# Optimization experiments

Hardware: AMD Instinct MI355X
Metric: run time of the kernel (lower is better)

Reference implementation:

```python
import jax, jax.numpy as jnp
import numpy as np

H = 4096      # hidden_size
F = 14336     # intermediate_size (ffn)
GS = 64       # HQQ group_size along axis 0 (output rows)
NB = 4        # nbits
T = 512       # tokens routed to this expert


def _make_qlinear(key, N, K):
    """Quantized weight of logical shape (N, K) = (out, in), HQQ axis=0 groups."""
    k1, k2, k3 = jax.random.split(key, 3)
    W_q = jax.random.randint(k1, (N, K), 0, 2 ** NB, dtype=jnp.int32)
    scale = jax.random.uniform(k2, (N // GS, K), dtype=jnp.float32) * 0.02 + 1e-3
    zero = jax.random.uniform(k3, (N // GS, K), dtype=jnp.float32) * (2.0 ** (NB - 1))
    return W_q, scale, zero


def setup_inputs() -> dict:
    key = jax.random.key(0)
    kx, k1, k2, k3 = jax.random.split(key, 4)
    w1_q, w1_scale, w1_zero = _make_qlinear(k1, F, H)  # gate proj
    w2_q, w2_scale, w2_zero = _make_qlinear(k2, H, F)  # down proj
    w3_q, w3_scale, w3_zero = _make_qlinear(k3, F, H)  # up proj
    hidden_states = jax.random.normal(kx, (T, H), dtype=jnp.float32)
    return dict(hidden_states=hidden_states,
                w1_q=w1_q, w1_scale=w1_scale, w1_zero=w1_zero,
                w2_q=w2_q, w2_scale=w2_scale, w2_zero=w2_zero,
                w3_q=w3_q, w3_scale=w3_scale, w3_zero=w3_zero)


def _dequant(W_q, scale, zero):
    # W[n, k] = (W_q[n, k] - zero[n // GS, k]) * scale[n // GS, k]
    N, K = W_q.shape
    Wf = W_q.reshape(N // GS, GS, K).astype(scale.dtype)
    return ((Wf - zero[:, None, :]) * scale[:, None, :]).reshape(N, K)


def reference(hidden_states,
              w1_q, w1_scale, w1_zero,
              w2_q, w2_scale, w2_zero,
              w3_q, w3_scale, w3_zero):
    gate = hidden_states @ _dequant(w1_q, w1_scale, w1_zero).T  # [T, F]
    up = hidden_states @ _dequant(w3_q, w3_scale, w3_zero).T    # [T, F]
    inter = jax.nn.silu(gate) * up                               # [T, F]
    return inter @ _dequant(w2_q, w2_scale, w2_zero).T           # [T, H]
```

## Files before the change

### kernel.cpp

```cpp
#include <hip/hip_runtime.h>
#include <stdint.h>

typedef __bf16 bf16;
typedef __attribute__((ext_vector_type(8))) bf16 bf16x8;
typedef __attribute__((ext_vector_type(4))) bf16 bf16x4;
typedef __attribute__((ext_vector_type(4))) float f32x4;

#define T_DIM 512
#define H_DIM 4096
#define F_DIM 14336

__device__ __forceinline__ int swz(int r, int c) {
    return r * 64 + (c ^ ((r & 7) << 3));
}

__device__ __forceinline__ int xcd_remap(int d, int chunk) {
    return (d & 7) * chunk + (d >> 3);
}

__device__ __forceinline__ void barrier_nodrain() {
    __builtin_amdgcn_sched_barrier(0);
    asm volatile("s_waitcnt lgkmcnt(0)\n\ts_barrier" ::: "memory");
    __builtin_amdgcn_sched_barrier(0);
}

__global__ void cvt_x_kernel(const float* __restrict__ x, bf16* __restrict__ xb) {
    int i = (blockIdx.x * 256 + threadIdx.x) * 4;
    float4 v = *(const float4*)(x + i);
    bf16x4 o = {(bf16)v.x, (bf16)v.y, (bf16)v.z, (bf16)v.w};
    *(bf16x4*)(xb + i) = o;
}

__global__ __launch_bounds__(256, 3)
void gemm_gateup(const bf16* __restrict__ A,
                 const int* __restrict__ Wq1, const float* __restrict__ Sc1,
                 const float* __restrict__ Zr1,
                 const int* __restrict__ Wq3, const float* __restrict__ Sc3,
                 const float* __restrict__ Zr3,
                 bf16* __restrict__ inter) {
    constexpr int KD = H_DIM;
    constexpr int NT = KD / 64;
    __shared__ __align__(16) bf16 As[2][128 * 64];
    __shared__ __align__(16) bf16 Bs1[2][32 * 64];
    __shared__ __align__(16) bf16 Bs3[2][32 * 64];

    const int l    = xcd_remap(blockIdx.x, 224);
    const int bx   = l & 3;
    const int by   = l >> 2;
    const int tid  = threadIdx.x;
    const int lane = tid & 63;
    const int wid  = tid >> 6;
    const int wm   = wid >> 1, wn = wid & 1;
    const int lr   = lane & 15;
    const int lk   = (lane >> 4) * 8;
    const int m0   = bx * 128;
    const int n0   = by * 32;
    const int grp  = n0 >> 6;

    const int a_r = tid >> 2;
    const int a_c = (tid & 3) * 8;
    const int b_r = (tid >> 4) * 2;
    const int b_c = (tid & 15) * 4;

    f32x4 acc1[4], acc3[4];
    const f32x4 zf = {0.f, 0.f, 0.f, 0.f};
#pragma unroll
    for (int i = 0; i < 4; i++) { acc1[i] = zf; acc3[i] = zf; }

    bf16x8 areg[4];
    int4   q1r[2], q3r[2];
    float4 s1r, z1r, s3r, z3r;

#define STAGE(K0)                                                                 \
    {                                                                             \
        _Pragma("unroll")                                                         \
        for (int p = 0; p < 2; p++)                                               \
            _Pragma("unroll")                                                     \
            for (int h = 0; h < 2; h++)                                           \
                areg[p * 2 + h] = *(const bf16x8*)(A + (size_t)(m0 + a_r + 64 * p) * KD + (K0) + a_c + 32 * h); \
        _Pragma("unroll")                                                         \
        for (int i = 0; i < 2; i++) {                                             \
            q1r[i] = *(const int4*)(Wq1 + (size_t)(n0 + b_r + i) * KD + (K0) + b_c); \
            q3r[i] = *(const int4*)(Wq3 + (size_t)(n0 + b_r + i) * KD + (K0) + b_c); \
        }                                                                         \
        s1r = *(const float4*)(Sc1 + (size_t)grp * KD + (K0) + b_c);              \
        z1r = *(const float4*)(Zr1 + (size_t)grp * KD + (K0) + b_c);              \
        s3r = *(const float4*)(Sc3 + (size_t)grp * KD + (K0) + b_c);              \
        z3r = *(const float4*)(Zr3 + (size_t)grp * KD + (K0) + b_c);              \
    }

#define WLDS(nb)                                                                  \
    {                                                                             \
        _Pragma("unroll")                                                         \
        for (int p = 0; p < 2; p++)                                               \
            _Pragma("unroll")                                                     \
            for (int h = 0; h < 2; h++)                                           \
                *(bf16x8*)&As[nb][swz(a_r + 64 * p, a_c + 32 * h)] = areg[p * 2 + h]; \
        float4 n1, n3;                                                            \
        n1.x = -z1r.x * s1r.x; n1.y = -z1r.y * s1r.y;                             \
        n1.z = -z1r.z * s1r.z; n1.w = -z1r.w * s1r.w;                             \
        n3.x = -z3r.x * s3r.x; n3.y = -z3r.y * s3r.y;                             \
        n3.z = -z3r.z * s3r.z; n3.w = -z3r.w * s3r.w;                             \
        _Pragma("unroll")                                                         \
        for (int i = 0; i < 2; i++) {                                             \
            bf16x4 v;                                                             \
            v[0] = (bf16)fmaf((float)q1r[i].x, s1r.x, n1.x);                      \
            v[1] = (bf16)fmaf((float)q1r[i].y, s1r.y, n1.y);                      \
            v[2] = (bf16)fmaf((float)q1r[i].z, s1r.z, n1.z);                      \
            v[3] = (bf16)fmaf((float)q1r[i].w, s1r.w, n1.w);                      \
            *(bf16x4*)&Bs1[nb][swz(b_r + i, b_c)] = v;                            \
            bf16x4 u;                                                             \
            u[0] = (bf16)fmaf((float)q3r[i].x, s3r.x, n3.x);                      \
            u[1] = (bf16)fmaf((float)q3r[i].y, s3r.y, n3.y);                      \
            u[2] = (bf16)fmaf((float)q3r[i].z, s3r.z, n3.z);                      \
            u[3] = (bf16)fmaf((float)q3r[i].w, s3r.w, n3.w);                      \
            *(bf16x4*)&Bs3[nb][swz(b_r + i, b_c)] = u;                            \
        }                                                                         \
    }

    STAGE(0);
    WLDS(0);
    STAGE(64);
    barrier_nodrain();

    for (int t = 0; t < NT; ++t) {
        const int cur = t & 1;
#pragma unroll
        for (int kk = 0; kk < 2; kk++) {
            bf16x8 af[4], b1, b3;
#pragma unroll
            for (int mi = 0; mi < 4; mi++)
                af[mi] = *(const bf16x8*)&As[cur][swz(wm * 64 + mi * 16 + lr, kk * 32 + lk)];
            b1 = *(const bf16x8*)&Bs1[cur][swz(wn * 16 + lr, kk * 32 + lk)];
            b3 = *(const bf16x8*)&Bs3[cur][swz(wn * 16 + lr, kk * 32 + lk)];
#pragma unroll
            for (int mi = 0; mi < 4; mi++) {
                acc1[mi] = __builtin_amdgcn_mfma_f32_16x16x32_bf16(af[mi], b1, acc1[mi], 0, 0, 0);
                acc3[mi] = __builtin_amdgcn_mfma_f32_16x16x32_bf16(af[mi], b3, acc3[mi], 0, 0, 0);
            }
        }
        if (t + 1 < NT) {
            WLDS(cur ^ 1);
            if (t + 2 < NT) STAGE((t + 2) * 64);
            barrier_nodrain();
        }
    }
#undef STAGE
#undef WLDS

    const int orow = (lane >> 4) * 4;
#pragma unroll
    for (int mi = 0; mi < 4; mi++) {
#pragma unroll
        for (int r = 0; r < 4; r++) {
            int m = m0 + wm * 64 + mi * 16 + orow + r;
            int c = n0 + wn * 16 + lr;
            float g = acc1[mi][r];
            float u = acc3[mi][r];
            float s = g / (1.0f + __expf(-g));
            inter[(size_t)m * F_DIM + c] = (bf16)(s * u);
        }
    }
}

template<int SPLITK>
__global__ __launch_bounds__(256, 4)
void gemm_down(const bf16* __restrict__ A, const int* __restrict__ Wq,
               const float* __restrict__ Sc, const float* __restrict__ Zr,
               float* __restrict__ partials) {
    constexpr int KD = F_DIM;
    constexpr int KC = KD / SPLITK;
    constexpr int NT = KC / 64;
    __shared__ __align__(16) bf16 As[2][128 * 64];
    __shared__ __align__(16) bf16 Bs[2][32 * 64];

    const int l    = xcd_remap(blockIdx.x, 64 * SPLITK);
    const int bx   = l & 3;
    const int by   = (l >> 2) & 127;
    const int bz   = l >> 9;
    const int tid  = threadIdx.x;
    const int lane = tid & 63;
    const int wid  = tid >> 6;
    const int wm   = wid >> 1, wn = wid & 1;
    const int lr   = lane & 15;
    const int lk   = (lane >> 4) * 8;
    const int m0   = bx * 128;
    const int n0   = by * 32;
    const int grp  = n0 >> 6;
    const int kbeg = bz * KC;

    const int a_r = tid >> 2;
    const int a_c = (tid & 3) * 8;
    const int b_r = (tid >> 4) * 2;
    const int b_c = (tid & 15) * 4;

    f32x4 acc[4];
    const f32x4 zf = {0.f, 0.f, 0.f, 0.f};
#pragma unroll
    for (int i = 0; i < 4; i++) acc[i] = zf;

    bf16x8 areg[4];
    int4   qr[2];
    float4 sr, zr;

#define STAGE(K0)                                                                 \
    {                                                                             \
        _Pragma("unroll")                                                         \
        for (int p = 0; p < 2; p++)                                               \
            _Pragma("unroll")                                                     \
            for (int h = 0; h < 2; h++)                                           \
                areg[p * 2 + h] = *(const bf16x8*)(A + (size_t)(m0 + a_r + 64 * p) * KD + kbeg + (K0) + a_c + 32 * h); \
        _Pragma("unroll")                                                         \
        for (int i = 0; i < 2; i++)                                               \
            qr[i] = *(const int4*)(Wq + (size_t)(n0 + b_r + i) * KD + kbeg + (K0) + b_c); \
        sr = *(const float4*)(Sc + (size_t)grp * KD + kbeg + (K0) + b_c);         \
        zr = *(const float4*)(Zr + (size_t)grp * KD + kbeg + (K0) + b_c);         \
    }

#define WLDS(nb)                                                                  \
    {                                                                             \
        _Pragma("unroll")                                                         \
        for (int p = 0; p < 2; p++)                                               \
            _Pragma("unroll")                                                     \
            for (int h = 0; h < 2; h++)                                           \
                *(bf16x8*)&As[nb][swz(a_r + 64 * p, a_c + 32 * h)] = areg[p * 2 + h]; \
        float4 nz;                                                                \
        nz.x = -zr.x * sr.x; nz.y = -zr.y * sr.y;                                 \
        nz.z = -zr.z * sr.z; nz.w = -zr.w * sr.w;                                 \
        _Pragma("unroll")                                                         \
        for (int i = 0; i < 2; i++) {                                             \
            bf16x4 v;                                                             \
            v[0] = (bf16)fmaf((float)qr[i].x, sr.x, nz.x);                        \
            v[1] = (bf16)fmaf((float)qr[i].y, sr.y, nz.y);                        \
            v[2] = (bf16)fmaf((float)qr[i].z, sr.z, nz.z);                        \
            v[3] = (bf16)fmaf((float)qr[i].w, sr.w, nz.w);                        \
            *(bf16x4*)&Bs[nb][swz(b_r + i, b_c)] = v;                             \
        }                                                                         \
    }

    STAGE(0);
    WLDS(0);
    STAGE(64);
    barrier_nodrain();

    for (int t = 0; t < NT; ++t) {
        const int cur = t & 1;
#pragma unroll
        for (int kk = 0; kk < 2; kk++) {
            bf16x8 af[4], bfr;
#pragma unroll
            for (int mi = 0; mi < 4; mi++)
                af[mi] = *(const bf16x8*)&As[cur][swz(wm * 64 + mi * 16 + lr, kk * 32 + lk)];
            bfr = *(const bf16x8*)&Bs[cur][swz(wn * 16 + lr, kk * 32 + lk)];
#pragma unroll
            for (int mi = 0; mi < 4; mi++)
                acc[mi] = __builtin_amdgcn_mfma_f32_16x16x32_bf16(af[mi], bfr, acc[mi], 0, 0, 0);
        }
        if (t + 1 < NT) {
            WLDS(cur ^ 1);
            if (t + 2 < NT) STAGE((t + 2) * 64);
            barrier_nodrain();
        }
    }
#undef STAGE
#undef WLDS

    float* po = partials + (size_t)bz * T_DIM * H_DIM;
    const int orow = (lane >> 4) * 4;
#pragma unroll
    for (int mi = 0; mi < 4; mi++) {
#pragma unroll
        for (int r = 0; r < 4; r++) {
            int m = m0 + wm * 64 + mi * 16 + orow + r;
            int c = n0 + wn * 16 + lr;
            po[(size_t)m * H_DIM + c] = acc[mi][r];
        }
    }
}

template<int S>
__global__ void reduce_kernel(const float* __restrict__ partials, float* __restrict__ out) {
    size_t i = ((size_t)blockIdx.x * 256 + threadIdx.x) * 4;
    f32x4 a = *(const f32x4*)(partials + i);
#pragma unroll
    for (int s = 1; s < S; s++)
        a += *(const f32x4*)(partials + (size_t)s * T_DIM * H_DIM + i);
    *(f32x4*)(out + i) = a;
}

extern "C" void kernel_launch(void* const* d_in, const int* in_sizes, int n_in,
                              void* d_out, int out_size, void* d_ws, size_t ws_size,
                              hipStream_t stream) {
    const float* x   = (const float*)d_in[0];
    const int*   w1q = (const int*)d_in[1];
    const float* w1s = (const float*)d_in[2];
    const float* w1z = (const float*)d_in[3];
    const int*   w2q = (const int*)d_in[4];
    const float* w2s = (const float*)d_in[5];
    const float* w2z = (const float*)d_in[6];
    const int*   w3q = (const int*)d_in[7];
    const float* w3s = (const float*)d_in[8];
    const float* w3z = (const float*)d_in[9];

    bf16*  xb    = (bf16*)d_ws;
    bf16*  inter = xb + (size_t)T_DIM * H_DIM;
    float* parts = (float*)(inter + (size_t)T_DIM * F_DIM);

    const size_t base   = (size_t)T_DIM * H_DIM * 2 + (size_t)T_DIM * F_DIM * 2;
    const size_t pbytes = (size_t)T_DIM * H_DIM * 4;

    cvt_x_kernel<<<dim3(2048), dim3(256), 0, stream>>>(x, xb);

    gemm_gateup<<<dim3(1792), dim3(256), 0, stream>>>(
        xb, w1q, w1s, w1z, w3q, w3s, w3z, inter);

    if (ws_size >= base + 4 * pbytes) {
        gemm_down<4><<<dim3(2048), dim3(256), 0, stream>>>(inter, w2q, w2s, w2z, parts);
        reduce_kernel<4><<<dim3(2048), dim3(256), 0, stream>>>(parts, (float*)d_out);
    } else if (ws_size >= base + 2 * pbytes) {
        gemm_down<2><<<dim3(1024), dim3(256), 0, stream>>>(inter, w2q, w2s, w2z, parts);
        reduce_kernel<2><<<dim3(2048), dim3(256), 0, stream>>>(parts, (float*)d_out);
    } else {
        gemm_down<1><<<dim3(512), dim3(256), 0, stream>>>(inter, w2q, w2s, w2z, parts);
        reduce_kernel<1><<<dim3(2048), dim3(256), 0, stream>>>(parts, (float*)d_out);
    }
}
```

Baseline: 446.4 us.

## Pre-tile activations and DMA A tiles directly to LDS with deeper weight prefetch

The bf16 activations and the intermediate tensor are now written in a pre-swizzled 128x64 tile layout, so each A tile can be copied straight into LDS with global_load_lds 16-byte DMA instead of going through registers. Weight loads are double-buffered in registers, prefetching two K-tiles ahead, and barriers wait on partial vmcnt counts. The aim is to cut VGPR staging and LDS write instructions for A and to hide more global-load latency. The cost is a strict dependence on the custom layout and on hand-counted vmcnt values, which are fragile if the compiler reorders loads.

```diff
diff --git a/kernel.cpp b/kernel.cpp
--- a/kernel.cpp
+++ b/kernel.cpp
@@ -18,18 +18,30 @@
     return (d & 7) * chunk + (d >> 3);
 }
 
-__device__ __forceinline__ void barrier_nodrain() {
-    __builtin_amdgcn_sched_barrier(0);
-    asm volatile("s_waitcnt lgkmcnt(0)\n\ts_barrier" ::: "memory");
-    __builtin_amdgcn_sched_barrier(0);
-}
-
-__global__ void cvt_x_kernel(const float* __restrict__ x, bf16* __restrict__ xb) {
+__device__ __forceinline__ void dma16(const void* g, void* l) {
+    __builtin_amdgcn_global_load_lds(
+        (const __attribute__((address_space(1))) void*)g,
+        (__attribute__((address_space(3))) void*)l, 16, 0, 0);
+}
+
+#define BARRIER_VM(N)                                                        \
+    {                                                                        \
+        __builtin_amdgcn_sched_barrier(0);                                   \
+        asm volatile("s_waitcnt vmcnt(" #N ") lgkmcnt(0)\n\ts_barrier" ::: "memory"); \
+        __builtin_amdgcn_sched_barrier(0);                                   \
+    }
+
+__global__ void cvt_x_kernel(const float* __restrict__ x, bf16* __restrict__ xbt) {
     int i = (blockIdx.x * 256 + threadIdx.x) * 4;
+    int m = i >> 12;
+    int c = i & 4095;
     float4 v = *(const float4*)(x + i);
     bf16x4 o = {(bf16)v.x, (bf16)v.y, (bf16)v.z, (bf16)v.w};
-    *(bf16x4*)(xb + i) = o;
-}
+    int p = m >> 7, rm = m & 127, kt = c >> 6, kc = c & 63;
+    *(bf16x4*)(xbt + (size_t)(p * 64 + kt) * 8192 + swz(rm, kc)) = o;
+}
+
+struct WSet { int4 q1[2], q3[2]; float4 s1, z1, s3, z3; };
 
 __global__ __launch_bounds__(256, 3)
 void gemm_gateup(const bf16* __restrict__ A,
@@ -57,115 +69,153 @@
     const int n0   = by * 32;
     const int grp  = n0 >> 6;
 
-    const int a_r = tid >> 2;
-    const int a_c = (tid & 3) * 8;
     const int b_r = (tid >> 4) * 2;
     const int b_c = (tid & 15) * 4;
 
+    const char*  atile = (const char*)A + (size_t)bx * 64 * 16384;
+    const size_t dmaoff = (size_t)wid * 4096 + lane * 16;
+
+    const int*   q1B = Wq1 + (size_t)(n0 + b_r) * KD + b_c;
+    const int*   q3B = Wq3 + (size_t)(n0 + b_r) * KD + b_c;
+    const float* s1B = Sc1 + (size_t)grp * KD + b_c;
+    const float* z1B = Zr1 + (size_t)grp * KD + b_c;
+    const float* s3B = Sc3 + (size_t)grp * KD + b_c;
+    const float* z3B = Zr3 + (size_t)grp * KD + b_c;
+
     f32x4 acc1[4], acc3[4];
     const f32x4 zf = {0.f, 0.f, 0.f, 0.f};
 #pragma unroll
     for (int i = 0; i < 4; i++) { acc1[i] = zf; acc3[i] = zf; }
 
-    bf16x8 areg[4];
-    int4   q1r[2], q3r[2];
-    float4 s1r, z1r, s3r, z3r;
-
-#define STAGE(K0)                                                                 \
-    {                                                                             \
-        _Pragma("unroll")                                                         \
-        for (int p = 0; p < 2; p++)                                               \
-            _Pragma("unroll")                                                     \
-            for (int h = 0; h < 2; h++)                                           \
-                areg[p * 2 + h] = *(const bf16x8*)(A + (size_t)(m0 + a_r + 64 * p) * KD + (K0) + a_c + 32 * h); \
-        _Pragma("unroll")                                                         \
-        for (int i = 0; i < 2; i++) {                                             \
-            q1r[i] = *(const int4*)(Wq1 + (size_t)(n0 + b_r + i) * KD + (K0) + b_c); \
-            q3r[i] = *(const int4*)(Wq3 + (size_t)(n0 + b_r + i) * KD + (K0) + b_c); \
-        }                                                                         \
-        s1r = *(const float4*)(Sc1 + (size_t)grp * KD + (K0) + b_c);              \
-        z1r = *(const float4*)(Zr1 + (size_t)grp * KD + (K0) + b_c);              \
-        s3r = *(const float4*)(Sc3 + (size_t)grp * KD + (K0) + b_c);              \
-        z3r = *(const float4*)(Zr3 + (size_t)grp * KD + (K0) + b_c);              \
-    }
-
-#define WLDS(nb)                                                                  \
-    {                                                                             \
-        _Pragma("unroll")                                                         \
-        for (int p = 0; p < 2; p++)                                               \
-            _Pragma("unroll")                                                     \
-            for (int h = 0; h < 2; h++)                                           \
-                *(bf16x8*)&As[nb][swz(a_r + 64 * p, a_c + 32 * h)] = areg[p * 2 + h]; \
-        float4 n1, n3;                                                            \
-        n1.x = -z1r.x * s1r.x; n1.y = -z1r.y * s1r.y;                             \
-        n1.z = -z1r.z * s1r.z; n1.w = -z1r.w * s1r.w;                             \
-        n3.x = -z3r.x * s3r.x; n3.y = -z3r.y * s3r.y;                             \
-        n3.z = -z3r.z * s3r.z; n3.w = -z3r.w * s3r.w;                             \
-        _Pragma("unroll")                                                         \
-        for (int i = 0; i < 2; i++) {                                             \
-            bf16x4 v;                                                             \
-            v[0] = (bf16)fmaf((float)q1r[i].x, s1r.x, n1.x);                      \
-            v[1] = (bf16)fmaf((float)q1r[i].y, s1r.y, n1.y);                      \
-            v[2] = (bf16)fmaf((float)q1r[i].z, s1r.z, n1.z);                      \
-            v[3] = (bf16)fmaf((float)q1r[i].w, s1r.w, n1.w);                      \
-            *(bf16x4*)&Bs1[nb][swz(b_r + i, b_c)] = v;                            \
-            bf16x4 u;                                                             \
-            u[0] = (bf16)fmaf((float)q3r[i].x, s3r.x, n3.x);                      \
-            u[1] = (bf16)fmaf((float)q3r[i].y, s3r.y, n3.y);                      \
-            u[2] = (bf16)fmaf((float)q3r[i].z, s3r.z, n3.z);                      \
-            u[3] = (bf16)fmaf((float)q3r[i].w, s3r.w, n3.w);                      \
-            *(bf16x4*)&Bs3[nb][swz(b_r + i, b_c)] = u;                            \
-        }                                                                         \
-    }
-
-    STAGE(0);
-    WLDS(0);
-    STAGE(64);
-    barrier_nodrain();
-
-    for (int t = 0; t < NT; ++t) {
-        const int cur = t & 1;
-#pragma unroll
-        for (int kk = 0; kk < 2; kk++) {
-            bf16x8 af[4], b1, b3;
-#pragma unroll
-            for (int mi = 0; mi < 4; mi++)
-                af[mi] = *(const bf16x8*)&As[cur][swz(wm * 64 + mi * 16 + lr, kk * 32 + lk)];
-            b1 = *(const bf16x8*)&Bs1[cur][swz(wn * 16 + lr, kk * 32 + lk)];
-            b3 = *(const bf16x8*)&Bs3[cur][swz(wn * 16 + lr, kk * 32 + lk)];
-#pragma unroll
-            for (int mi = 0; mi < 4; mi++) {
-                acc1[mi] = __builtin_amdgcn_mfma_f32_16x16x32_bf16(af[mi], b1, acc1[mi], 0, 0, 0);
-                acc3[mi] = __builtin_amdgcn_mfma_f32_16x16x32_bf16(af[mi], b3, acc3[mi], 0, 0, 0);
+    WSet sA, sB;
+
+#define GU_DMA(TILE, nb)                                                      \
+    {                                                                         \
+        const char* _s = atile + (size_t)(TILE) * 16384 + dmaoff;             \
+        char* _d = (char*)&As[nb][0] + wid * 4096;                            \
+        _Pragma("unroll")                                                     \
+        for (int j = 0; j < 4; j++) dma16(_s + j * 1024, _d + j * 1024);      \
+    }
+
+#define GU_STAGE(S, K0)                                                       \
+    {                                                                         \
+        _Pragma("unroll")                                                     \
+        for (int i = 0; i < 2; i++) {                                         \
+            S.q1[i] = *(const int4*)(q1B + (size_t)i * KD + (K0));            \
+            S.q3[i] = *(const int4*)(q3B + (size_t)i * KD + (K0));            \
+        }                                                                     \
+        S.s1 = *(const float4*)(s1B + (K0));                                  \
+        S.z1 = *(const float4*)(z1B + (K0));                                  \
+        S.s3 = *(const float4*)(s3B + (K0));                                  \
+        S.z3 = *(const float4*)(z3B + (K0));                                  \
+    }
+
+#define GU_WLDS(S, nb)                                                        \
+    {                                                                         \
+        float4 n1, n3;                                                        \
+        n1.x = -S.z1.x * S.s1.x; n1.y = -S.z1.y * S.s1.y;                     \
+        n1.z = -S.z1.z * S.s1.z; n1.w = -S.z1.w * S.s1.w;                     \
+        n3.x = -S.z3.x * S.s3.x; n3.y = -S.z3.y * S.s3.y;                     \
+        n3.z = -S.z3.z * S.s3.z; n3.w = -S.z3.w * S.s3.w;                     \
+        _Pragma("unroll")                                                     \
+        for (int i = 0; i < 2; i++) {                                         \
+            bf16x4 v;                                                         \
+            v[0] = (bf16)fmaf((float)S.q1[i].x, S.s1.x, n1.x);                \
+            v[1] = (bf16)fmaf((float)S.q1[i].y, S.s1.y, n1.y);                \
+            v[2] = (bf16)fmaf((float)S.q1[i].z, S.s1.z, n1.z);                \
+            v[3] = (bf16)fmaf((float)S.q1[i].w, S.s1.w, n1.w);                \
+            *(bf16x4*)&Bs1[nb][swz(b_r + i, b_c)] = v;                        \
+            bf16x4 u;                                                         \
+            u[0] = (bf16)fmaf((float)S.q3[i].x, S.s3.x, n3.x);                \
+            u[1] = (bf16)fmaf((float)S.q3[i].y, S.s3.y, n3.y);                \
+            u[2] = (bf16)fmaf((float)S.q3[i].z, S.s3.z, n3.z);                \
+            u[3] = (bf16)fmaf((float)S.q3[i].w, S.s3.w, n3.w);                \
+            *(bf16x4*)&Bs3[nb][swz(b_r + i, b_c)] = u;                        \
+        }                                                                     \
+    }
+
+#define GU_MFMA(nb)                                                           \
+    {                                                                         \
+        _Pragma("unroll")                                                     \
+        for (int kk = 0; kk < 2; kk++) {                                      \
+            bf16x8 af[4], b1, b3;                                             \
+            _Pragma("unroll")                                                 \
+            for (int mi = 0; mi < 4; mi++)                                    \
+                af[mi] = *(const bf16x8*)&As[nb][swz(wm * 64 + mi * 16 + lr, kk * 32 + lk)]; \
+            b1 = *(const bf16x8*)&Bs1[nb][swz(wn * 16 + lr, kk * 32 + lk)];   \
+            b3 = *(const bf16x8*)&Bs3[nb][swz(wn * 16 + lr, kk * 32 + lk)];   \
+            _Pragma("unroll")                                                 \
+            for (int mi = 0; mi < 4; mi++) {                                  \
+                acc1[mi] = __builtin_amdgcn_mfma_f32_16x16x32_bf16(af[mi], b1, acc1[mi], 0, 0, 0); \
+                acc3[mi] = __builtin_amdgcn_mfma_f32_16x16x32_bf16(af[mi], b3, acc3[mi], 0, 0, 0); \
+            }                                                                 \
+        }                                                                     \
+    }
+
+    GU_STAGE(sA, 0);
+    GU_DMA(0, 0);
+    GU_WLDS(sA, 0);
+    GU_STAGE(sB, 64);
+    GU_STAGE(sA, 128);
+    BARRIER_VM(16);
+
+    for (int t = 0; t < NT; t += 2) {
+        if (t + 1 < NT) GU_DMA(t + 1, 1);
+        __builtin_amdgcn_sched_barrier(0);
+        GU_MFMA(0);
+        if (t + 1 < NT) {
+            GU_WLDS(sB, 1);
+            if (t + 3 < NT) {
+                GU_STAGE(sB, (t + 3) * 64);
+                BARRIER_VM(8);
+            } else {
+                BARRIER_VM(0);
             }
         }
-        if (t + 1 < NT) {
-            WLDS(cur ^ 1);
-            if (t + 2 < NT) STAGE((t + 2) * 64);
-            barrier_nodrain();
-        }
-    }
-#undef STAGE
-#undef WLDS
+        const int u = t + 1;
+        if (u < NT) {
+            if (u + 1 < NT) GU_DMA(u + 1, 0);
+            __builtin_amdgcn_sched_barrier(0);
+            GU_MFMA(1);
+            if (u + 1 < NT) {
+                GU_WLDS(sA, 0);
+                if (u + 3 < NT) {
+                    GU_STAGE(sA, (u + 3) * 64);
+                    BARRIER_VM(8);
+                } else {
+                    BARRIER_VM(0);
+                }
+            }
+        }
+    }
+#undef GU_DMA
+#undef GU_STAGE
+#undef GU_WLDS
+#undef GU_MFMA
 
     const int orow = (lane >> 4) * 4;
+    const int cg   = n0 + wn * 16 + lr;
+    const int kt   = cg >> 6, kc = cg & 63;
+    bf16* itile = inter + (size_t)(bx * 224 + kt) * 8192;
 #pragma unroll
     for (int mi = 0; mi < 4; mi++) {
 #pragma unroll
         for (int r = 0; r < 4; r++) {
-            int m = m0 + wm * 64 + mi * 16 + orow + r;
-            int c = n0 + wn * 16 + lr;
+            int rm = (wm * 64 + mi * 16 + orow + r) & 127;
             float g = acc1[mi][r];
             float u = acc3[mi][r];
             float s = g / (1.0f + __expf(-g));
-            inter[(size_t)m * F_DIM + c] = (bf16)(s * u);
-        }
-    }
-}
+            itile[swz(rm, kc)] = (bf16)(s * u);
+        }
+    }
+}
+
+struct WSetD { int4 q[2]; float4 s, z; };
 
 template<int SPLITK>
 __global__ __launch_bounds__(256, 4)
-void gemm_down(const bf16* __restrict__ A, const int* __restrict__ Wq,
+void gemm_down(const bf16* __restrict__ A,
+               const int* __restrict__ Wq,
                const float* __restrict__ Sc, const float* __restrict__ Zr,
                float* __restrict__ partials) {
     constexpr int KD = F_DIM;
@@ -187,83 +237,114 @@
     const int m0   = bx * 128;
     const int n0   = by * 32;
     const int grp  = n0 >> 6;
-    const int kbeg = bz * KC;
-
-    const int a_r = tid >> 2;
-    const int a_c = (tid & 3) * 8;
+    const int kt0  = bz * (KC / 64);
+
     const int b_r = (tid >> 4) * 2;
     const int b_c = (tid & 15) * 4;
 
+    const char*  atile = (const char*)A + (size_t)(bx * 224 + kt0) * 16384;
+    const size_t dmaoff = (size_t)wid * 4096 + lane * 16;
+    const int    kbeg  = bz * KC;
+
+    const int*   qB = Wq + (size_t)(n0 + b_r) * KD + kbeg + b_c;
+    const float* sB_ = Sc + (size_t)grp * KD + kbeg + b_c;
+    const float* zB_ = Zr + (size_t)grp * KD + kbeg + b_c;
+
     f32x4 acc[4];
     const f32x4 zf = {0.f, 0.f, 0.f, 0.f};
 #pragma unroll
     for (int i = 0; i < 4; i++) acc[i] = zf;
 
-    bf16x8 areg[4];
-    int4   qr[2];
-    float4 sr, zr;
-
-#define STAGE(K0)                                                                 \
-    {                                                                             \
-        _Pragma("unroll")                                                         \
-        for (int p = 0; p < 2; p++)                                               \
-            _Pragma("unroll")                                                     \
-            for (int h = 0; h < 2; h++)                                           \
-                areg[p * 2 + h] = *(const bf16x8*)(A + (size_t)(m0 + a_r + 64 * p) * KD + kbeg + (K0) + a_c + 32 * h); \
-        _Pragma("unroll")                                                         \
-        for (int i = 0; i < 2; i++)                                               \
-            qr[i] = *(const int4*)(Wq + (size_t)(n0 + b_r + i) * KD + kbeg + (K0) + b_c); \
-        sr = *(const float4*)(Sc + (size_t)grp * KD + kbeg + (K0) + b_c);         \
-        zr = *(const float4*)(Zr + (size_t)grp * KD + kbeg + (K0) + b_c);         \
-    }
-
-#define WLDS(nb)                                                                  \
-    {                                                                             \
-        _Pragma("unroll")                                                         \
-        for (int p = 0; p < 2; p++)                                               \
-            _Pragma("unroll")                                                     \
-            for (int h = 0; h < 2; h++)                                           \
-                *(bf16x8*)&As[nb][swz(a_r + 64 * p, a_c + 32 * h)] = areg[p * 2 + h]; \
-        float4 nz;                                                                \
-        nz.x = -zr.x * sr.x; nz.y = -zr.y * sr.y;                                 \
-        nz.z = -zr.z * sr.z; nz.w = -zr.w * sr.w;                                 \
-        _Pragma("unroll")                                                         \
-        for (int i = 0; i < 2; i++) {                                             \
-            bf16x4 v;                                                             \
-            v[0] = (bf16)fmaf((float)qr[i].x, sr.x, nz.x);                        \
-            v[1] = (bf16)fmaf((float)qr[i].y, sr.y, nz.y);                        \
-            v[2] = (bf16)fmaf((float)qr[i].z, sr.z, nz.z);                        \
-            v[3] = (bf16)fmaf((float)qr[i].w, sr.w, nz.w);                        \
-            *(bf16x4*)&Bs[nb][swz(b_r + i, b_c)] = v;                             \
-        }                                                                         \
-    }
-
-    STAGE(0);
-    WLDS(0);
-    STAGE(64);
-    barrier_nodrain();
-
-    for (int t = 0; t < NT; ++t) {
-        const int cur = t & 1;
-#pragma unroll
-        for (int kk = 0; kk < 2; kk++) {
-            bf16x8 af[4], bfr;
-#pragma unroll
-            for (int mi = 0; mi < 4; mi++)
-                af[mi] = *(const bf16x8*)&As[cur][swz(wm * 64 + mi * 16 + lr, kk * 32 + lk)];
-            bfr = *(const bf16x8*)&Bs[cur][swz(wn * 16 + lr, kk * 32 + lk)];
-#pragma unroll
-            for (int mi = 0; mi < 4; mi++)
-                acc[mi] = __builtin_amdgcn_mfma_f32_16x16x32_bf16(af[mi], bfr, acc[mi], 0, 0, 0);
-        }
+    WSetD sA, sB;
+
+#define GD_DMA(TILE, nb)                                                      \
+    {                                                                         \
+        const char* _s = atile + (size_t)(TILE) * 16384 + dmaoff;             \
+        char* _d = (char*)&As[nb][0] + wid * 4096;                            \
+        _Pragma("unroll")                                                     \
+        for (int j = 0; j < 4; j++) dma16(_s + j * 1024, _d + j * 1024);      \
+    }
+
+#define GD_STAGE(S, K0)                                                       \
+    {                                                                         \
+        _Pragma("unroll")                                                     \
+        for (int i = 0; i < 2; i++)                                           \
+            S.q[i] = *(const int4*)(qB + (size_t)i * KD + (K0));              \
+        S.s = *(const float4*)(sB_ + (K0));                                   \
+        S.z = *(const float4*)(zB_ + (K0));                                   \
+    }
+
+#define GD_WLDS(S, nb)                                                        \
+    {                                                                         \
+        float4 nz;                                                            \
+        nz.x = -S.z.x * S.s.x; nz.y = -S.z.y * S.s.y;                         \
+        nz.z = -S.z.z * S.s.z; nz.w = -S.z.w * S.s.w;                         \
+        _Pragma("unroll")                                                     \
+        for (int i = 0; i < 2; i++) {                                         \
+            bf16x4 v;                                                         \
+            v[0] = (bf16)fmaf((float)S.q[i].x, S.s.x, nz.x);                  \
+            v[1] = (bf16)fmaf((float)S.q[i].y, S.s.y, nz.y);                  \
+            v[2] = (bf16)fmaf((float)S.q[i].z, S.s.z, nz.z);                  \
+            v[3] = (bf16)fmaf((float)S.q[i].w, S.s.w, nz.w);                  \
+            *(bf16x4*)&Bs[nb][swz(b_r + i, b_c)] = v;                         \
+        }                                                                     \
+    }
+
+#define GD_MFMA(nb)                                                           \
+    {                                                                         \
+        _Pragma("unroll")                                                     \
+        for (int kk = 0; kk < 2; kk++) {                                      \
+            bf16x8 af[4], bfr;                                                \
+            _Pragma("unroll")                                                 \
+            for (int mi = 0; mi < 4; mi++)                                    \
+                af[mi] = *(const bf16x8*)&As[nb][swz(wm * 64 + mi * 16 + lr, kk * 32 + lk)]; \
+            bfr = *(const bf16x8*)&Bs[nb][swz(wn * 16 + lr, kk * 32 + lk)];   \
+            _Pragma("unroll")                                                 \
+            for (int mi = 0; mi < 4; mi++)                                    \
+                acc[mi] = __builtin_amdgcn_mfma_f32_16x16x32_bf16(af[mi], bfr, acc[mi], 0, 0, 0); \
+        }                                                                     \
+    }
+
+    GD_STAGE(sA, 0);
+    GD_DMA(0, 0);
+    GD_WLDS(sA, 0);
+    GD_STAGE(sB, 64);
+    GD_STAGE(sA, 128);
+    BARRIER_VM(8);
+
+    for (int t = 0; t < NT; t += 2) {
+        if (t + 1 < NT) GD_DMA(t + 1, 1);
+        __builtin_amdgcn_sched_barrier(0);
+        GD_MFMA(0);
         if (t + 1 < NT) {
-            WLDS(cur ^ 1);
-            if (t + 2 < NT) STAGE((t + 2) * 64);
-            barrier_nodrain();
-        }
-    }
-#undef STAGE
-#undef WLDS
+            GD_WLDS(sB, 1);
+            if (t + 3 < NT) {
+                GD_STAGE(sB, (t + 3) * 64);
+                BARRIER_VM(4);
+            } else {
+                BARRIER_VM(0);
+            }
+        }
+        const int u = t + 1;
+        if (u < NT) {
+            if (u + 1 < NT) GD_DMA(u + 1, 0);
+            __builtin_amdgcn_sched_barrier(0);
+            GD_MFMA(1);
+            if (u + 1 < NT) {
+                GD_WLDS(sA, 0);
+                if (u + 3 < NT) {
+                    GD_STAGE(sA, (u + 3) * 64);
+                    BARRIER_VM(4);
+                } else {
+                    BARRIER_VM(0);
+                }
+            }
+        }
+    }
+#undef GD_DMA
+#undef GD_STAGE
+#undef GD_WLDS
+#undef GD_MFMA
 
     float* po = partials + (size_t)bz * T_DIM * H_DIM;
     const int orow = (lane >> 4) * 4;
```

Result: no change. 453.7 us (+1.6%).

## Pre-tile activations into swizzled tiles and read A fragments directly from global

Applied to the files above, without the earlier changes.

The bf16 activations and the intermediate tensor are now written into a pre-tiled, pre-swizzled layout of 128x64 tiles. Both GEMMs then load their A fragments directly from global memory instead of staging them through shared memory. This removes the A tile staging (global to register to LDS) and shrinks LDS use, which could raise occupancy. The trade-off is that every wave issues direct global loads in the inner loop with no LDS reuse across the two N-waves, so the kernel relies on L1/L2 caching and the loads may stall the MFMA pipeline.

```diff
diff --git a/kernel.cpp b/kernel.cpp
--- a/kernel.cpp
+++ b/kernel.cpp
@@ -24,11 +24,14 @@
     __builtin_amdgcn_sched_barrier(0);
 }
 
-__global__ void cvt_x_kernel(const float* __restrict__ x, bf16* __restrict__ xb) {
+__global__ void cvt_x_kernel(const float* __restrict__ x, bf16* __restrict__ xbt) {
     int i = (blockIdx.x * 256 + threadIdx.x) * 4;
+    int m = i >> 12;
+    int c = i & 4095;
     float4 v = *(const float4*)(x + i);
     bf16x4 o = {(bf16)v.x, (bf16)v.y, (bf16)v.z, (bf16)v.w};
-    *(bf16x4*)(xb + i) = o;
+    int p = m >> 7, rm = m & 127, kt = c >> 6, kc = c & 63;
+    *(bf16x4*)(xbt + (size_t)(p * 64 + kt) * 8192 + swz(rm, kc)) = o;
 }
 
 __global__ __launch_bounds__(256, 3)
@@ -40,7 +43,6 @@
                  bf16* __restrict__ inter) {
     constexpr int KD = H_DIM;
     constexpr int NT = KD / 64;
-    __shared__ __align__(16) bf16 As[2][128 * 64];
     __shared__ __align__(16) bf16 Bs1[2][32 * 64];
     __shared__ __align__(16) bf16 Bs3[2][32 * 64];
 
@@ -53,31 +55,24 @@
     const int wm   = wid >> 1, wn = wid & 1;
     const int lr   = lane & 15;
     const int lk   = (lane >> 4) * 8;
-    const int m0   = bx * 128;
     const int n0   = by * 32;
     const int grp  = n0 >> 6;
 
-    const int a_r = tid >> 2;
-    const int a_c = (tid & 3) * 8;
     const int b_r = (tid >> 4) * 2;
     const int b_c = (tid & 15) * 4;
 
+    const bf16* at0 = A + (size_t)bx * 64 * 8192;
+
     f32x4 acc1[4], acc3[4];
     const f32x4 zf = {0.f, 0.f, 0.f, 0.f};
 #pragma unroll
     for (int i = 0; i < 4; i++) { acc1[i] = zf; acc3[i] = zf; }
 
-    bf16x8 areg[4];
     int4   q1r[2], q3r[2];
     float4 s1r, z1r, s3r, z3r;
 
 #define STAGE(K0)                                                                 \
     {                                                                             \
-        _Pragma("unroll")                                                         \
-        for (int p = 0; p < 2; p++)                                               \
-            _Pragma("unroll")                                                     \
-            for (int h = 0; h < 2; h++)                                           \
-                areg[p * 2 + h] = *(const bf16x8*)(A + (size_t)(m0 + a_r + 64 * p) * KD + (K0) + a_c + 32 * h); \
         _Pragma("unroll")                                                         \
         for (int i = 0; i < 2; i++) {                                             \
             q1r[i] = *(const int4*)(Wq1 + (size_t)(n0 + b_r + i) * KD + (K0) + b_c); \
@@ -91,11 +86,6 @@
 
 #define WLDS(nb)                                                                  \
     {                                                                             \
-        _Pragma("unroll")                                                         \
-        for (int p = 0; p < 2; p++)                                               \
-            _Pragma("unroll")                                                     \
-            for (int h = 0; h < 2; h++)                                           \
-                *(bf16x8*)&As[nb][swz(a_r + 64 * p, a_c + 32 * h)] = areg[p * 2 + h]; \
         float4 n1, n3;                                                            \
         n1.x = -z1r.x * s1r.x; n1.y = -z1r.y * s1r.y;                             \
         n1.z = -z1r.z * s1r.z; n1.w = -z1r.w * s1r.w;                             \
@@ -125,12 +115,13 @@
 
     for (int t = 0; t < NT; ++t) {
         const int cur = t & 1;
+        const bf16* at = at0 + (size_t)t * 8192;
 #pragma unroll
         for (int kk = 0; kk < 2; kk++) {
             bf16x8 af[4], b1, b3;
 #pragma unroll
             for (int mi = 0; mi < 4; mi++)
-                af[mi] = *(const bf16x8*)&As[cur][swz(wm * 64 + mi * 16 + lr, kk * 32 + lk)];
+                af[mi] = *(const bf16x8*)(at + swz(wm * 64 + mi * 16 + lr, kk * 32 + lk));
             b1 = *(const bf16x8*)&Bs1[cur][swz(wn * 16 + lr, kk * 32 + lk)];
             b3 = *(const bf16x8*)&Bs3[cur][swz(wn * 16 + lr, kk * 32 + lk)];
 #pragma unroll
@@ -149,29 +140,31 @@
 #undef WLDS
 
     const int orow = (lane >> 4) * 4;
+    const int cg   = n0 + wn * 16 + lr;
+    const int kt   = cg >> 6, kc = cg & 63;
+    bf16* itile = inter + (size_t)(bx * 224 + kt) * 8192;
 #pragma unroll
     for (int mi = 0; mi < 4; mi++) {
 #pragma unroll
         for (int r = 0; r < 4; r++) {
-            int m = m0 + wm * 64 + mi * 16 + orow + r;
-            int c = n0 + wn * 16 + lr;
+            int rm = wm * 64 + mi * 16 + orow + r;
             float g = acc1[mi][r];
             float u = acc3[mi][r];
             float s = g / (1.0f + __expf(-g));
-            inter[(size_t)m * F_DIM + c] = (bf16)(s * u);
+            itile[swz(rm, kc)] = (bf16)(s * u);
         }
     }
 }
 
 template<int SPLITK>
 __global__ __launch_bounds__(256, 4)
-void gemm_down(const bf16* __restrict__ A, const int* __restrict__ Wq,
+void gemm_down(const bf16* __restrict__ A,
+               const int* __restrict__ Wq,
                const float* __restrict__ Sc, const float* __restrict__ Zr,
                float* __restrict__ partials) {
     constexpr int KD = F_DIM;
     constexpr int KC = KD / SPLITK;
     constexpr int NT = KC / 64;
-    __shared__ __align__(16) bf16 As[2][128 * 64];
     __shared__ __align__(16) bf16 Bs[2][32 * 64];
 
     const int l    = xcd_remap(blockIdx.x, 64 * SPLITK);
@@ -189,27 +182,21 @@
     const int grp  = n0 >> 6;
     const int kbeg = bz * KC;
 
-    const int a_r = tid >> 2;
-    const int a_c = (tid & 3) * 8;
     const int b_r = (tid >> 4) * 2;
     const int b_c = (tid & 15) * 4;
 
+    const bf16* at0 = A + (size_t)(bx * 224 + bz * NT) * 8192;
+
     f32x4 acc[4];
     const f32x4 zf = {0.f, 0.f, 0.f, 0.f};
 #pragma unroll
     for (int i = 0; i < 4; i++) acc[i] = zf;
 
-    bf16x8 areg[4];
     int4   qr[2];
     float4 sr, zr;
 
 #define STAGE(K0)                                                                 \
     {                                                                             \
-        _Pragma("unroll")                                                         \
-        for (int p = 0; p < 2; p++)                                               \
-            _Pragma("unroll")                                                     \
-            for (int h = 0; h < 2; h++)                                           \
-                areg[p * 2 + h] = *(const bf16x8*)(A + (size_t)(m0 + a_r + 64 * p) * KD + kbeg + (K0) + a_c + 32 * h); \
         _Pragma("unroll")                                                         \
         for (int i = 0; i < 2; i++)                                               \
             qr[i] = *(const int4*)(Wq + (size_t)(n0 + b_r + i) * KD + kbeg + (K0) + b_c); \
@@ -219,11 +206,6 @@
 
 #define WLDS(nb)                                                                  \
     {                                                                             \
-        _Pragma("unroll")                                                         \
-        for (int p = 0; p < 2; p++)                                               \
-            _Pragma("unroll")                                                     \
-            for (int h = 0; h < 2; h++)                                           \
-                *(bf16x8*)&As[nb][swz(a_r + 64 * p, a_c + 32 * h)] = areg[p * 2 + h]; \
         float4 nz;                                                                \
         nz.x = -zr.x * sr.x; nz.y = -zr.y * sr.y;                                 \
         nz.z = -zr.z * sr.z; nz.w = -zr.w * sr.w;                                 \
@@ -245,16 +227,17 @@
 
     for (int t = 0; t < NT; ++t) {
         const int cur = t & 1;
+        const bf16* at = at0 + (size_t)t * 8192;
 #pragma unroll
         for (int kk = 0; kk < 2; kk++) {
-            bf16x8 af[4], bfr;
+            bf16x8 af[4], bv;
 #pragma unroll
             for (int mi = 0; mi < 4; mi++)
-                af[mi] = *(const bf16x8*)&As[cur][swz(wm * 64 + mi * 16 + lr, kk * 32 + lk)];
-            bfr = *(const bf16x8*)&Bs[cur][swz(wn * 16 + lr, kk * 32 + lk)];
+                af[mi] = *(const bf16x8*)(at + swz(wm * 64 + mi * 16 + lr, kk * 32 + lk));
+            bv = *(const bf16x8*)&Bs[cur][swz(wn * 16 + lr, kk * 32 + lk)];
 #pragma unroll
             for (int mi = 0; mi < 4; mi++)
-                acc[mi] = __builtin_amdgcn_mfma_f32_16x16x32_bf16(af[mi], bfr, acc[mi], 0, 0, 0);
+                acc[mi] = __builtin_amdgcn_mfma_f32_16x16x32_bf16(af[mi], bv, acc[mi], 0, 0, 0);
         }
         if (t + 1 < NT) {
             WLDS(cur ^ 1);
```

Measured after the change: 627.2 us. 1.41x slower.

## Widen N tile to 64 in gate/up and down GEMMs

Applied to the files above, without the earlier changes.

Both dequant GEMMs now compute a 128x64 output tile per block instead of 128x32, with each wave holding a 4x2 grid of MFMA accumulators and reading two B fragments per k-step. This halves the number of blocks and the redundant loads of the activation (A) tile per unit of output. It also lets one scale/zero group row cover the whole tile. In exchange it uses more registers and LDS per block, so launch bounds drop (3→2 and 4→3 blocks per CU) and grids shrink (896 and 1024 blocks), which lowers occupancy and latency hiding.

```diff
diff --git a/kernel.cpp b/kernel.cpp
--- a/kernel.cpp
+++ b/kernel.cpp
@@ -31,7 +31,7 @@
     *(bf16x4*)(xb + i) = o;
 }
 
-__global__ __launch_bounds__(256, 3)
+__global__ __launch_bounds__(256, 2)
 void gemm_gateup(const bf16* __restrict__ A,
                  const int* __restrict__ Wq1, const float* __restrict__ Sc1,
                  const float* __restrict__ Zr1,
@@ -41,10 +41,10 @@
     constexpr int KD = H_DIM;
     constexpr int NT = KD / 64;
     __shared__ __align__(16) bf16 As[2][128 * 64];
-    __shared__ __align__(16) bf16 Bs1[2][32 * 64];
-    __shared__ __align__(16) bf16 Bs3[2][32 * 64];
-
-    const int l    = xcd_remap(blockIdx.x, 224);
+    __shared__ __align__(16) bf16 Bs1[2][64 * 64];
+    __shared__ __align__(16) bf16 Bs3[2][64 * 64];
+
+    const int l    = xcd_remap(blockIdx.x, 112);
     const int bx   = l & 3;
     const int by   = l >> 2;
     const int tid  = threadIdx.x;
@@ -54,21 +54,23 @@
     const int lr   = lane & 15;
     const int lk   = (lane >> 4) * 8;
     const int m0   = bx * 128;
-    const int n0   = by * 32;
-    const int grp  = n0 >> 6;
+    const int n0   = by * 64;
+    const int grp  = by;
 
     const int a_r = tid >> 2;
     const int a_c = (tid & 3) * 8;
-    const int b_r = (tid >> 4) * 2;
+    const int b_r = (tid >> 4) * 4;
     const int b_c = (tid & 15) * 4;
 
-    f32x4 acc1[4], acc3[4];
+    f32x4 acc1[4][2], acc3[4][2];
     const f32x4 zf = {0.f, 0.f, 0.f, 0.f};
 #pragma unroll
-    for (int i = 0; i < 4; i++) { acc1[i] = zf; acc3[i] = zf; }
+    for (int i = 0; i < 4; i++)
+#pragma unroll
+        for (int j = 0; j < 2; j++) { acc1[i][j] = zf; acc3[i][j] = zf; }
 
     bf16x8 areg[4];
-    int4   q1r[2], q3r[2];
+    int4   q1r[4], q3r[4];
     float4 s1r, z1r, s3r, z3r;
 
 #define STAGE(K0)                                                                 \
@@ -79,7 +81,7 @@
             for (int h = 0; h < 2; h++)                                           \
                 areg[p * 2 + h] = *(const bf16x8*)(A + (size_t)(m0 + a_r + 64 * p) * KD + (K0) + a_c + 32 * h); \
         _Pragma("unroll")                                                         \
-        for (int i = 0; i < 2; i++) {                                             \
+        for (int i = 0; i < 4; i++) {                                             \
             q1r[i] = *(const int4*)(Wq1 + (size_t)(n0 + b_r + i) * KD + (K0) + b_c); \
             q3r[i] = *(const int4*)(Wq3 + (size_t)(n0 + b_r + i) * KD + (K0) + b_c); \
         }                                                                         \
@@ -102,7 +104,7 @@
         n3.x = -z3r.x * s3r.x; n3.y = -z3r.y * s3r.y;                             \
         n3.z = -z3r.z * s3r.z; n3.w = -z3r.w * s3r.w;                             \
         _Pragma("unroll")                                                         \
-        for (int i = 0; i < 2; i++) {                                             \
+        for (int i = 0; i < 4; i++) {                                             \
             bf16x4 v;                                                             \
             v[0] = (bf16)fmaf((float)q1r[i].x, s1r.x, n1.x);                      \
             v[1] = (bf16)fmaf((float)q1r[i].y, s1r.y, n1.y);                      \
@@ -127,17 +129,22 @@
         const int cur = t & 1;
 #pragma unroll
         for (int kk = 0; kk < 2; kk++) {
-            bf16x8 af[4], b1, b3;
+            bf16x8 af[4], b1[2], b3[2];
 #pragma unroll
             for (int mi = 0; mi < 4; mi++)
                 af[mi] = *(const bf16x8*)&As[cur][swz(wm * 64 + mi * 16 + lr, kk * 32 + lk)];
-            b1 = *(const bf16x8*)&Bs1[cur][swz(wn * 16 + lr, kk * 32 + lk)];
-            b3 = *(const bf16x8*)&Bs3[cur][swz(wn * 16 + lr, kk * 32 + lk)];
-#pragma unroll
-            for (int mi = 0; mi < 4; mi++) {
-                acc1[mi] = __builtin_amdgcn_mfma_f32_16x16x32_bf16(af[mi], b1, acc1[mi], 0, 0, 0);
-                acc3[mi] = __builtin_amdgcn_mfma_f32_16x16x32_bf16(af[mi], b3, acc3[mi], 0, 0, 0);
+#pragma unroll
+            for (int ni = 0; ni < 2; ni++) {
+                b1[ni] = *(const bf16x8*)&Bs1[cur][swz(wn * 32 + ni * 16 + lr, kk * 32 + lk)];
+                b3[ni] = *(const bf16x8*)&Bs3[cur][swz(wn * 32 + ni * 16 + lr, kk * 32 + lk)];
             }
+#pragma unroll
+            for (int mi = 0; mi < 4; mi++)
+#pragma unroll
+                for (int ni = 0; ni < 2; ni++) {
+                    acc1[mi][ni] = __builtin_amdgcn_mfma_f32_16x16x32_bf16(af[mi], b1[ni], acc1[mi][ni], 0, 0, 0);
+                    acc3[mi][ni] = __builtin_amdgcn_mfma_f32_16x16x32_bf16(af[mi], b3[ni], acc3[mi][ni], 0, 0, 0);
+                }
         }
         if (t + 1 < NT) {
             WLDS(cur ^ 1);
@@ -150,21 +157,23 @@
 
     const int orow = (lane >> 4) * 4;
 #pragma unroll
-    for (int mi = 0; mi < 4; mi++) {
-#pragma unroll
-        for (int r = 0; r < 4; r++) {
-            int m = m0 + wm * 64 + mi * 16 + orow + r;
-            int c = n0 + wn * 16 + lr;
-            float g = acc1[mi][r];
-            float u = acc3[mi][r];
-            float s = g / (1.0f + __expf(-g));
-            inter[(size_t)m * F_DIM + c] = (bf16)(s * u);
-        }
-    }
+    for (int mi = 0; mi < 4; mi++)
+#pragma unroll
+        for (int ni = 0; ni < 2; ni++) {
+#pragma unroll
+            for (int r = 0; r < 4; r++) {
+                int m = m0 + wm * 64 + mi * 16 + orow + r;
+                int c = n0 + wn * 32 + ni * 16 + lr;
+                float g = acc1[mi][ni][r];
+                float u = acc3[mi][ni][r];
+                float s = g / (1.0f + __expf(-g));
+                inter[(size_t)m * F_DIM + c] = (bf16)(s * u);
+            }
+        }
 }
 
 template<int SPLITK>
-__global__ __launch_bounds__(256, 4)
+__global__ __launch_bounds__(256, 3)
 void gemm_down(const bf16* __restrict__ A, const int* __restrict__ Wq,
                const float* __restrict__ Sc, const float* __restrict__ Zr,
                float* __restrict__ partials) {
@@ -172,12 +181,12 @@
     constexpr int KC = KD / SPLITK;
     constexpr int NT = KC / 64;
     __shared__ __align__(16) bf16 As[2][128 * 64];
-    __shared__ __align__(16) bf16 Bs[2][32 * 64];
-
-    const int l    = xcd_remap(blockIdx.x, 64 * SPLITK);
+    __shared__ __align__(16) bf16 Bs[2][64 * 64];
+
+    const int l    = xcd_remap(blockIdx.x, 32 * SPLITK);
     const int bx   = l & 3;
-    const int by   = (l >> 2) & 127;
-    const int bz   = l >> 9;
+    const int by   = (l >> 2) & 63;
+    const int bz   = l >> 8;
     const int tid  = threadIdx.x;
     const int lane = tid & 63;
     const int wid  = tid >> 6;
@@ -185,22 +194,24 @@
     const int lr   = lane & 15;
     const int lk   = (lane >> 4) * 8;
     const int m0   = bx * 128;
-    const int n0   = by * 32;
-    const int grp  = n0 >> 6;
+    const int n0   = by * 64;
+    const int grp  = by;
     const int kbeg = bz * KC;
 
     const int a_r = tid >> 2;
     const int a_c = (tid & 3) * 8;
-    const int b_r = (tid >> 4) * 2;
+    const int b_r = (tid >> 4) * 4;
     const int b_c = (tid & 15) * 4;
 
-    f32x4 acc[4];
+    f32x4 acc[4][2];
     const f32x4 zf = {0.f, 0.f, 0.f, 0.f};
 #pragma unroll
-    for (int i = 0; i < 4; i++) acc[i] = zf;
+    for (int i = 0; i < 4; i++)
+#pragma unroll
+        for (int j = 0; j < 2; j++) acc[i][j] = zf;
 
     bf16x8 areg[4];
-    int4   qr[2];
+    int4   qr[4];
     float4 sr, zr;
 
 #define STAGE(K0)                                                                 \
@@ -211,7 +222,7 @@
             for (int h = 0; h < 2; h++)                                           \
                 areg[p * 2 + h] = *(const bf16x8*)(A + (size_t)(m0 + a_r + 64 * p) * KD + kbeg + (K0) + a_c + 32 * h); \
         _Pragma("unroll")                                                         \
-        for (int i = 0; i < 2; i++)                                               \
+        for (int i = 0; i < 4; i++)                                               \
             qr[i] = *(const int4*)(Wq + (size_t)(n0 + b_r + i) * KD + kbeg + (K0) + b_c); \
         sr = *(const float4*)(Sc + (size_t)grp * KD + kbeg + (K0) + b_c);         \
         zr = *(const float4*)(Zr + (size_t)grp * KD + kbeg + (K0) + b_c);         \
@@ -228,7 +239,7 @@
         nz.x = -zr.x * sr.x; nz.y = -zr.y * sr.y;                                 \
         nz.z = -zr.z * sr.z; nz.w = -zr.w * sr.w;                                 \
         _Pragma("unroll")                                                         \
-        for (int i = 0; i < 2; i++) {                                             \
+        for (int i = 0; i < 4; i++) {                                             \
             bf16x4 v;                                                             \
             v[0] = (bf16)fmaf((float)qr[i].x, sr.x, nz.x);                        \
             v[1] = (bf16)fmaf((float)qr[i].y, sr.y, nz.y);                        \
@@ -247,14 +258,18 @@
         const int cur = t & 1;
 #pragma unroll
         for (int kk = 0; kk < 2; kk++) {
-            bf16x8 af[4], bfr;
+            bf16x8 af[4], bfr[2];
 #pragma unroll
             for (int mi = 0; mi < 4; mi++)
                 af[mi] = *(const bf16x8*)&As[cur][swz(wm * 64 + mi * 16 + lr, kk * 32 + lk)];
-            bfr = *(const bf16x8*)&Bs[cur][swz(wn * 16 + lr, kk * 32 + lk)];
+#pragma unroll
+            for (int ni = 0; ni < 2; ni++)
+                bfr[ni] = *(const bf16x8*)&Bs[cur][swz(wn * 32 + ni * 16 + lr, kk * 32 + lk)];
 #pragma unroll
             for (int mi = 0; mi < 4; mi++)
-                acc[mi] = __builtin_amdgcn_mfma_f32_16x16x32_bf16(af[mi], bfr, acc[mi], 0, 0, 0);
+#pragma unroll
+                for (int ni = 0; ni < 2; ni++)
+                    acc[mi][ni] = __builtin_amdgcn_mfma_f32_16x16x32_bf16(af[mi], bfr[ni], acc[mi][ni], 0, 0, 0);
         }
         if (t + 1 < NT) {
             WLDS(cur ^ 1);
@@ -268,14 +283,16 @@
     float* po = partials + (size_t)bz * T_DIM * H_DIM;
     const int orow = (lane >> 4) * 4;
 #pragma unroll
-    for (int mi = 0; mi < 4; mi++) {
-#pragma unroll
-        for (int r = 0; r < 4; r++) {
-            int m = m0 + wm * 64 + mi * 16 + orow + r;
-            int c = n0 + wn * 16 + lr;
-            po[(size_t)m * H_DIM + c] = acc[mi][r];
-        }
-    }
+    for (int mi = 0; mi < 4; mi++)
+#pragma unroll
+        for (int ni = 0; ni < 2; ni++) {
+#pragma unroll
+            for (int r = 0; r < 4; r++) {
+                int m = m0 + wm * 64 + mi * 16 + orow + r;
+                int c = n0 + wn * 32 + ni * 16 + lr;
+                po[(size_t)m * H_DIM + c] = acc[mi][ni][r];
+            }
+        }
 }
 
 template<int S>
@@ -311,17 +328,17 @@
 
     cvt_x_kernel<<<dim3(2048), dim3(256), 0, stream>>>(x, xb);
 
-    gemm_gateup<<<dim3(1792), dim3(256), 0, stream>>>(
+    gemm_gateup<<<dim3(896), dim3(256), 0, stream>>>(
         xb, w1q, w1s, w1z, w3q, w3s, w3z, inter);
 
     if (ws_size >= base + 4 * pbytes) {
-        gemm_down<4><<<dim3(2048), dim3(256), 0, stream>>>(inter, w2q, w2s, w2z, parts);
+        gemm_down<4><<<dim3(1024), dim3(256), 0, stream>>>(inter, w2q, w2s, w2z, parts);
         reduce_kernel<4><<<dim3(2048), dim3(256), 0, stream>>>(parts, (float*)d_out);
     } else if (ws_size >= base + 2 * pbytes) {
-        gemm_down<2><<<dim3(1024), dim3(256), 0, stream>>>(inter, w2q, w2s, w2z, parts);
+        gemm_down<2><<<dim3(512), dim3(256), 0, stream>>>(inter, w2q, w2s, w2z, parts);
         reduce_kernel<2><<<dim3(2048), dim3(256), 0, stream>>>(parts, (float*)d_out);
     } else {
-        gemm_down<1><<<dim3(512), dim3(256), 0, stream>>>(inter, w2q, w2s, w2z, parts);
+        gemm_down<1><<<dim3(256), dim3(256), 0, stream>>>(inter, w2q, w2s, w2z, parts);
         reduce_kernel<1><<<dim3(2048), dim3(256), 0, stream>>>(parts, (float*)d_out);
     }
 }
```

Measured after the change: 381.4 us. -14.5%, faster.
